# Optimization experiments

Hardware: AMD Instinct MI355X
Metric: run time of the kernel (lower is better)

The kernel has to match this reference:

```python
import jax, jax.numpy as jnp
import numpy as np

B, N, E, D = 8, 10000, 160000, 256
H = D // 2
SLOPE = 0.2  # LeakyReLU negative slope


def setup_inputs() -> dict:
    key = jax.random.key(0)
    ks = jax.random.split(key, 8)
    node_feats = jax.random.normal(ks[0], (B, N, D), dtype=jnp.float32)
    edge_attr = jax.random.uniform(ks[1], (E, 1), dtype=jnp.float32)
    W1 = jax.random.normal(ks[2], (2 * D, H), dtype=jnp.float32) * 0.05
    b1 = jnp.zeros((H,), dtype=jnp.float32)
    W2 = jax.random.normal(ks[3], (H, 1), dtype=jnp.float32) * 0.05
    b2 = jnp.zeros((1,), dtype=jnp.float32)
    edge_index = jax.random.randint(ks[4], (2, E), 0, N, dtype=jnp.int64)
    valid_masks = jax.random.randint(ks[5], (B, N), 0, 2).astype(bool)
    return {"node_feats": node_feats, "edge_attr": edge_attr, "W1": W1, "b1": b1,
            "W2": W2, "b2": b2, "edge_index": edge_index, "valid_masks": valid_masks}


def reference(node_feats, edge_attr, W1, b1, W2, b2, edge_index, valid_masks):
    # node_feats: [B,N,D]; edge_index: [2,E] shared across batch
    d = node_feats.shape[-1]
    src, dst = edge_index[0], edge_index[1]
    # cat([src_feats, dst_feats]) @ W1 == src @ W1[:d] + dst @ W1[d:]
    # Project per-node first, then gather per-edge: avoids the [B,E,2D] concat.
    ps = jnp.einsum('bnd,dh->bnh', node_feats, W1[:d])   # [B,N,H]
    pd = jnp.einsum('bnd,dh->bnh', node_feats, W1[d:])   # [B,N,H]
    h = ps[:, src] + pd[:, dst] + b1                      # [B,E,H]
    h = jnp.where(h >= 0, h, SLOPE * h)                   # LeakyReLU(0.2)
    scores = jnp.einsum('beh,h->be', h, W2[:, 0]) + b2[0]  # [B,E]
    scores = scores * edge_attr[:, 0]                     # edge_attr multiplies pre-softmax
    w = jax.nn.softmax(scores, axis=1)                    # global softmax over all edges
    # sparse_coo(edge_index, w) @ node_feats: out[src[e]] += w[e] * feats[dst[e]]
    msg = w[..., None] * node_feats[:, dst]               # [B,E,D]
    n = node_feats.shape[1]
    agg = jax.vmap(lambda m: jax.ops.segment_sum(m, src, num_segments=n))(msg)  # [B,N,D]
    mask = valid_masks.astype(node_feats.dtype)           # [B,N]
    cnt = mask.sum(axis=1)                                # [B]
    masked_mean = (agg * mask[..., None]).sum(axis=1) / jnp.maximum(cnt, 1.0)[:, None]
    full_mean = agg.mean(axis=1)
    graph_feats = jnp.where((cnt > 0)[:, None], masked_mean, full_mean)  # [B,D]
    return graph_feats, w
```

## Files before the change

### kernel.cpp

```cpp
#include <hip/hip_runtime.h>
#include <hip/hip_bf16.h>
#include <hip/hip_fp16.h>

#define B_ 8
#define N_ 10000
#define E_ 160000
#define D_ 256
#define H_ 128
#define SLOPE 0.2f
#define NCHUNK 50

#define EC_ 16
#define NR_ 32
#define RANGE_ 320
#define NPAD_ (NR_ * RANGE_)

#define NB_ 64
#define EPB_ (E_ / NB_)
#define BINS_ 256
#define NPB_ (N_ / 16)

#define SB_ 64
#define SEB_ (E_ / SB_)

typedef __attribute__((ext_vector_type(8))) _Float16 v8h;
typedef __attribute__((ext_vector_type(4))) _Float16 v4h;
typedef __attribute__((ext_vector_type(2))) _Float16 v2h;
typedef __attribute__((ext_vector_type(4))) float f32x4;

static __device__ __forceinline__ float dot2f(v2h a, v2h b, float c) {
#if __has_builtin(__builtin_amdgcn_fdot2)
    return __builtin_amdgcn_fdot2(a, b, c, false);
#else
    return fmaf((float)a.y, (float)b.y, fmaf((float)a.x, (float)b.x, c));
#endif
}

__global__ __launch_bounds__(64) void k_detect(const int* __restrict__ eidx_raw,
                                               const unsigned int* __restrict__ mask32,
                                               int* __restrict__ flags) {
    const int t = threadIdx.x;
    unsigned long long oddnz = __ballot(eidx_raw[2 * t + 1] != 0);
    unsigned long long mgt1  = __ballot(mask32[t] > 1u);
    if (t == 0) {
        flags[0] = (oddnz == 0ull) ? 1 : 0;
        flags[1] = (mgt1 != 0ull) ? 1 : 0;
    }
}

__global__ __launch_bounds__(256) void k_canon(const int* __restrict__ eidx_raw,
                                               const unsigned char* __restrict__ mask8,
                                               const unsigned int* __restrict__ mask32,
                                               const int* __restrict__ flags,
                                               const float* __restrict__ W1,
                                               const float* __restrict__ b1,
                                               const float* __restrict__ W2,
                                               int* __restrict__ ce,
                                               unsigned char* __restrict__ cm,
                                               unsigned char* __restrict__ cmT,
                                               __half* __restrict__ Wt,
                                               __half* __restrict__ b1h,
                                               __half* __restrict__ w2h) {
    const int i = blockIdx.x * 256 + threadIdx.x;
    const int f_e = flags[0], f_m = flags[1];
    if (i < 2 * E_) ce[i] = f_e ? eidx_raw[2 * i] : eidx_raw[i];
    if (i < B_ * N_) {
        unsigned char v = f_m ? (unsigned char)(mask8[i] != 0)
                              : (unsigned char)(mask32[i] != 0u);
        cm[i] = v;
        const int b = i / N_;
        const int n = i - b * N_;
        cmT[n * 8 + b] = v;
    }
    if (i < 2 * 256 * 128) {
        const int f = i & 127;
        const int row = i >> 7;
        const int c = row >> 8, k = row & 255;
        Wt[((c * 128 + f) * 256) + k] = __float2half(W1[row * 128 + f]);
    }
    if (i < 128) {
        b1h[i] = __float2half(b1[i]);
        w2h[i] = __float2half(W2[i]);
    }
}

__global__ __launch_bounds__(256) void khist(const int* __restrict__ ce,
                                             const unsigned char* __restrict__ cm,
                                             int* __restrict__ hpart,
                                             float* __restrict__ cnt) {
    const int tid = threadIdx.x;
    if (blockIdx.x < NB_) {
        __shared__ int h[BINS_];
        h[tid] = 0;
        __syncthreads();
        const int base = blockIdx.x * EPB_;
        for (int i = tid; i < EPB_; i += 256) {
            const int s = ce[base + i], d = ce[E_ + base + i];
            const int bin = (d / NPB_) * 16 + s / NPB_;
            atomicAdd(&h[bin], 1);
        }
        __syncthreads();
        hpart[blockIdx.x * BINS_ + tid] = h[tid];
    } else {
        const int b = blockIdx.x - NB_;
        int c = 0;
        for (int i = tid; i < N_; i += 256) c += cm[b * N_ + i] ? 1 : 0;
        __shared__ int red[256];
        red[tid] = c;
        __syncthreads();
        for (int s = 128; s > 0; s >>= 1) {
            if (tid < s) red[tid] += red[tid + s];
            __syncthreads();
        }
        if (tid == 0) cnt[b] = (float)red[0];
    }
}

__global__ __launch_bounds__(256) void kprefix(const int* __restrict__ hpart,
                                               int* __restrict__ offsetG) {
    __shared__ int cnt[BINS_];
    __shared__ int excl[BINS_];
    const int bin = threadIdx.x;
    int c = 0;
    for (int b = 0; b < NB_; b++) c += hpart[b * BINS_ + bin];
    cnt[bin] = c;
    __syncthreads();
    if (bin == 0) {
        int r = 0;
        for (int i = 0; i < BINS_; i++) { excl[i] = r; r += cnt[i]; }
    }
    __syncthreads();
    int run = excl[bin];
    for (int b = 0; b < NB_; b++) {
        offsetG[b * BINS_ + bin] = run;
        run += hpart[b * BINS_ + bin];
    }
}

__global__ __launch_bounds__(256) void kscatter(const int* __restrict__ ce,
                                                const int* __restrict__ offsetG,
                                                int* __restrict__ srcS,
                                                int* __restrict__ dstS,
                                                int* __restrict__ origS,
                                                int* __restrict__ rank) {
    __shared__ int loc[BINS_];
    const int tid = threadIdx.x;
    loc[tid] = offsetG[blockIdx.x * BINS_ + tid];
    __syncthreads();
    const int base = blockIdx.x * EPB_;
    for (int i = tid; i < EPB_; i += 256) {
        const int e = base + i;
        const int s = ce[e], d = ce[E_ + e];
        const int bin = (d / NPB_) * 16 + s / NPB_;
        const int pos = atomicAdd(&loc[bin], 1);
        srcS[pos] = s;
        dstS[pos] = d;
        origS[pos] = e;
        rank[e] = pos;
    }
}

__global__ __launch_bounds__(256) void k1_mfma(const float* __restrict__ X,
                                               const __half* __restrict__ Wt,
                                               __half* __restrict__ ps,
                                               __half* __restrict__ pd) {
    const int rb = blockIdx.x;
    const int tid = threadIdx.x;
    const int wave = tid >> 6, lane = tid & 63;
    const int quad = lane >> 4, l16 = lane & 15;

    __shared__ _Float16 Xs[128 * 40];

    f32x4 acc[2][2][8];
#pragma unroll
    for (int c = 0; c < 2; c++)
#pragma unroll
        for (int i = 0; i < 2; i++)
#pragma unroll
            for (int j = 0; j < 8; j++) acc[c][i][j] = (f32x4){0.f, 0.f, 0.f, 0.f};

    const int row_base = rb * 128;
    const int sr = tid >> 1;
    const int sh = tid & 1;

    for (int kc = 0; kc < 8; ++kc) {
        {
            const float4* src = (const float4*)&X[(size_t)(row_base + sr) * 256 + kc * 32 + sh * 16];
            _Float16* dst = &Xs[sr * 40 + sh * 16];
#pragma unroll
            for (int j = 0; j < 4; ++j) {
                float4 v = src[j];
                v4h p = {(_Float16)v.x, (_Float16)v.y, (_Float16)v.z, (_Float16)v.w};
                *(v4h*)&dst[j * 4] = p;
            }
        }
        __syncthreads();

        v8h wf[2][2];
#pragma unroll
        for (int cb = 0; cb < 2; ++cb)
#pragma unroll
            for (int ft = 0; ft < 2; ++ft)
                wf[cb][ft] = *(const v8h*)&Wt[((size_t)cb * 128 + wave * 32 + ft * 16 + l16) * 256 + kc * 32 + quad * 8];

#pragma unroll
        for (int nt = 0; nt < 8; ++nt) {
            v8h xf = *(v8h*)&Xs[(nt * 16 + l16) * 40 + quad * 8];
            acc[0][0][nt] = __builtin_amdgcn_mfma_f32_16x16x32_f16(wf[0][0], xf, acc[0][0][nt], 0, 0, 0);
            acc[0][1][nt] = __builtin_amdgcn_mfma_f32_16x16x32_f16(wf[0][1], xf, acc[0][1][nt], 0, 0, 0);
            acc[1][0][nt] = __builtin_amdgcn_mfma_f32_16x16x32_f16(wf[1][0], xf, acc[1][0][nt], 0, 0, 0);
            acc[1][1][nt] = __builtin_amdgcn_mfma_f32_16x16x32_f16(wf[1][1], xf, acc[1][1][nt], 0, 0, 0);
        }
        __syncthreads();
    }

#pragma unroll
    for (int nt = 0; nt < 8; ++nt) {
        const int R = row_base + nt * 16 + l16;
        const int b = R / N_;
        const int n = R - b * N_;
        const size_t off = ((size_t)(n * 8 + b)) * 128 + wave * 32 + quad * 4;
#pragma unroll
        for (int cb = 0; cb < 2; ++cb) {
            __half* base = (cb ? pd : ps) + off;
#pragma unroll
            for (int ft = 0; ft < 2; ++ft) {
                f32x4 a = acc[cb][ft][nt];
                v4h h = {(_Float16)a.x, (_Float16)a.y, (_Float16)a.z, (_Float16)a.w};
                *(v4h*)(base + ft * 16) = h;
            }
        }
    }
}

__global__ __launch_bounds__(256) void k2_scores(const __half* __restrict__ ps,
                                                 const __half* __restrict__ pd,
                                                 const int* __restrict__ srcS,
                                                 const int* __restrict__ dstS,
                                                 const int* __restrict__ origS,
                                                 const __half* __restrict__ b1h,
                                                 const __half* __restrict__ w2h,
                                                 const float* __restrict__ b2,
                                                 const float* __restrict__ eattr,
                                                 float* __restrict__ scS) {
    const int tid = threadIdx.x;
    const int wave = tid >> 6;
    const int lane = tid & 63;
    const int bid = blockIdx.x;
    const int lb = (bid & 7) * 5000 + (bid >> 3);
    const int e = lb * 4 + wave;

    const int b = lane >> 3;
    const int hi = (lane & 7) * 16;

    v2h b1p[8], w2p[8];
    {
        const v2h* bp = (const v2h*)(b1h + hi);
        const v2h* wp = (const v2h*)(w2h + hi);
#pragma unroll
        for (int j = 0; j < 8; j++) { b1p[j] = bp[j]; w2p[j] = wp[j]; }
    }

    const int src = srcS[e];
    const int dst = dstS[e];
    const int orig = origS[e];

    const float4* aps = (const float4*)&ps[((size_t)src * 8 + b) * 128 + hi];
    const float4* apd = (const float4*)&pd[((size_t)dst * 8 + b) * 128 + hi];
    float4 rs[2] = {aps[0], aps[1]};
    float4 rd[2] = {apd[0], apd[1]};
    const v2h* sv = (const v2h*)rs;
    const v2h* dv = (const v2h*)rd;

    const v2h slp = {(_Float16)SLOPE, (_Float16)SLOPE};
    float acc = 0.f;
#pragma unroll
    for (int j = 0; j < 8; j++) {
        v2h x = sv[j] + dv[j] + b1p[j];
        v2h l = __builtin_elementwise_max(x, x * slp);
        acc = dot2f(l, w2p[j], acc);
    }
    acc += __shfl_xor(acc, 1);
    acc += __shfl_xor(acc, 2);
    acc += __shfl_xor(acc, 4);

    if ((lane & 7) == 0) {
        scS[(size_t)e * 8 + b] = (acc + b2[0]) * eattr[orig];
    }
}

__global__ __launch_bounds__(256) void k3a_max(const float* __restrict__ scS,
                                               float* __restrict__ pmax) {
    const int tid = threadIdx.x;
    const int wave = tid >> 6, lane = tid & 63;
    const int base = blockIdx.x * SEB_;
    float fm[8];
#pragma unroll
    for (int j = 0; j < 8; j++) fm[j] = -3.4e38f;
    for (int i = tid; i < SEB_; i += 256) {
        const float4* s4 = (const float4*)&scS[(size_t)(base + i) * 8];
        float4 a = s4[0], b = s4[1];
        fm[0] = fmaxf(fm[0], a.x); fm[1] = fmaxf(fm[1], a.y);
        fm[2] = fmaxf(fm[2], a.z); fm[3] = fmaxf(fm[3], a.w);
        fm[4] = fmaxf(fm[4], b.x); fm[5] = fmaxf(fm[5], b.y);
        fm[6] = fmaxf(fm[6], b.z); fm[7] = fmaxf(fm[7], b.w);
    }
#pragma unroll
    for (int k = 1; k <= 32; k <<= 1)
#pragma unroll
        for (int j = 0; j < 8; j++) fm[j] = fmaxf(fm[j], __shfl_xor(fm[j], k));
    __shared__ float lmax[4][8];
    if (lane == 0)
#pragma unroll
        for (int j = 0; j < 8; j++) lmax[wave][j] = fm[j];
    __syncthreads();
    if (tid < 8) {
        float v = fmaxf(fmaxf(lmax[0][tid], lmax[1][tid]), fmaxf(lmax[2][tid], lmax[3][tid]));
        pmax[blockIdx.x * 8 + tid] = v;
    }
}

__global__ __launch_bounds__(256) void k3c_sum(const float* __restrict__ scS,
                                               const float* __restrict__ pmax,
                                               double* __restrict__ psum) {
    const int tid = threadIdx.x;
    const int wave = tid >> 6, lane = tid & 63;
    __shared__ float sm[8];
    if (tid < SB_) {
        float v[8];
        const float4* p4 = (const float4*)&pmax[tid * 8];
        float4 a = p4[0], b = p4[1];
        v[0] = a.x; v[1] = a.y; v[2] = a.z; v[3] = a.w;
        v[4] = b.x; v[5] = b.y; v[6] = b.z; v[7] = b.w;
#pragma unroll
        for (int k = 1; k <= 32; k <<= 1)
#pragma unroll
            for (int j = 0; j < 8; j++) v[j] = fmaxf(v[j], __shfl_xor(v[j], k));
        if (tid == 0)
#pragma unroll
            for (int j = 0; j < 8; j++) sm[j] = v[j];
    }
    __syncthreads();
    float m[8];
#pragma unroll
    for (int j = 0; j < 8; j++) m[j] = sm[j];

    const int base = blockIdx.x * SEB_;
    double s[8];
#pragma unroll
    for (int j = 0; j < 8; j++) s[j] = 0.0;
    for (int i = tid; i < SEB_; i += 256) {
        const float4* s4 = (const float4*)&scS[(size_t)(base + i) * 8];
        float4 a = s4[0], b = s4[1];
        s[0] += (double)expf(a.x - m[0]); s[1] += (double)expf(a.y - m[1]);
        s[2] += (double)expf(a.z - m[2]); s[3] += (double)expf(a.w - m[3]);
        s[4] += (double)expf(b.x - m[4]); s[5] += (double)expf(b.y - m[5]);
        s[6] += (double)expf(b.z - m[6]); s[7] += (double)expf(b.w - m[7]);
    }
#pragma unroll
    for (int k = 1; k <= 32; k <<= 1)
#pragma unroll
        for (int j = 0; j < 8; j++) s[j] += __shfl_xor(s[j], k);
    __shared__ double lsum[4][8];
    if (lane == 0)
#pragma unroll
        for (int j = 0; j < 8; j++) lsum[wave][j] = s[j];
    __syncthreads();
    if (tid < 8) {
        psum[blockIdx.x * 8 + tid] = lsum[0][tid] + lsum[1][tid] + lsum[2][tid] + lsum[3][tid];
    }
}

__global__ __launch_bounds__(256) void k3e_norm(const float* __restrict__ scS,
                                                const int* __restrict__ rank,
                                                const float* __restrict__ pmax,
                                                const double* __restrict__ psum,
                                                float* __restrict__ wout,
                                                float* __restrict__ wT) {
    const int tid = threadIdx.x;
    __shared__ float smx[8], sinvx[8];
    if (tid < 64) {
        float v[8];
        const float4* p4 = (const float4*)&pmax[tid * 8];
        float4 a = p4[0], b = p4[1];
        v[0] = a.x; v[1] = a.y; v[2] = a.z; v[3] = a.w;
        v[4] = b.x; v[5] = b.y; v[6] = b.z; v[7] = b.w;
#pragma unroll
        for (int k = 1; k <= 32; k <<= 1)
#pragma unroll
            for (int j = 0; j < 8; j++) v[j] = fmaxf(v[j], __shfl_xor(v[j], k));
        if (tid == 0)
#pragma unroll
            for (int j = 0; j < 8; j++) smx[j] = v[j];
    } else if (tid < 128) {
        const int l = tid - 64;
        double s[8];
#pragma unroll
        for (int j = 0; j < 8; j++) s[j] = psum[l * 8 + j];
#pragma unroll
        for (int k = 1; k <= 32; k <<= 1)
#pragma unroll
            for (int j = 0; j < 8; j++) s[j] += __shfl_xor(s[j], k);
        if (l == 0)
#pragma unroll
            for (int j = 0; j < 8; j++) sinvx[j] = (float)(1.0 / s[j]);
    }
    __syncthreads();

    const int e = blockIdx.x * 256 + tid;
    const int p = rank[e];
    const float4* s4 = (const float4*)&scS[(size_t)p * 8];
    float4 a = s4[0], b = s4[1];
    float wv[8];
    wv[0] = expf(a.x - smx[0]) * sinvx[0]; wv[1] = expf(a.y - smx[1]) * sinvx[1];
    wv[2] = expf(a.z - smx[2]) * sinvx[2]; wv[3] = expf(a.w - smx[3]) * sinvx[3];
    wv[4] = expf(b.x - smx[4]) * sinvx[4]; wv[5] = expf(b.y - smx[5]) * sinvx[5];
    wv[6] = expf(b.z - smx[6]) * sinvx[6]; wv[7] = expf(b.w - smx[7]) * sinvx[7];
#pragma unroll
    for (int j = 0; j < 8; j++) wout[(size_t)j * E_ + e] = wv[j];
    *(float4*)&wT[(size_t)e * 8]     = make_float4(wv[0], wv[1], wv[2], wv[3]);
    *(float4*)&wT[(size_t)e * 8 + 4] = make_float4(wv[4], wv[5], wv[6], wv[7]);
}

__global__ __launch_bounds__(256) void k3f_bin(const int* __restrict__ ce,
                                               const float* __restrict__ wT,
                                               const unsigned char* __restrict__ cmT,
                                               float* __restrict__ Wpart) {
    const int ec = blockIdx.x;
    const int rg = blockIdx.y;
    const int n0 = rg * RANGE_;

    __shared__ float lWf[RANGE_ * 8];
    __shared__ float lWm[RANGE_ * 8];
    for (int i = threadIdx.x; i < RANGE_ * 8; i += 256) { lWf[i] = 0.f; lWm[i] = 0.f; }
    __syncthreads();

    const int4* dst4 = (const int4*)(ce + E_);
    const int base4 = ec * (E_ / EC_ / 4);
    for (int i = threadIdx.x; i < E_ / EC_ / 4; i += 256) {
        int4 d4 = dst4[base4 + i];
        int dd[4] = {d4.x, d4.y, d4.z, d4.w};
        const int e0 = (base4 + i) * 4;
#pragma unroll
        for (int j = 0; j < 4; ++j) {
            const int rel = dd[j] - n0;
            if ((unsigned)rel < (unsigned)RANGE_) {
                const int e = e0 + j;
                const int src = ce[e];
                float4 w0 = *(const float4*)&wT[(size_t)e * 8];
                float4 w1 = *(const float4*)&wT[(size_t)e * 8 + 4];
                const unsigned long long mm = *(const unsigned long long*)&cmT[src * 8];
                float wv[8] = {w0.x, w0.y, w0.z, w0.w, w1.x, w1.y, w1.z, w1.w};
                float* lf = &lWf[rel * 8];
                float* lm = &lWm[rel * 8];
#pragma unroll
                for (int b = 0; b < 8; b++) {
                    atomicAdd(&lf[b], wv[b]);
                    if ((mm >> (8 * b)) & 1ull) atomicAdd(&lm[b], wv[b]);
                }
            }
        }
    }
    __syncthreads();

    float* of = Wpart + ((size_t)ec * 2 + 0) * (NPAD_ * 8) + n0 * 8;
    float* om = Wpart + ((size_t)ec * 2 + 1) * (NPAD_ * 8) + n0 * 8;
    for (int i = threadIdx.x; i < RANGE_ * 8; i += 256) { of[i] = lWf[i]; om[i] = lWm[i]; }
}

__global__ __launch_bounds__(256) void k3g_reduce(const float* __restrict__ Wpart,
                                                  float* __restrict__ WfT,
                                                  float* __restrict__ WmT) {
    const int i = blockIdx.x * 256 + threadIdx.x;
    float sf = 0.f, sm = 0.f;
#pragma unroll
    for (int ec = 0; ec < EC_; ec++) {
        sf += Wpart[(size_t)ec * 2 * (NPAD_ * 8) + i];
        sm += Wpart[((size_t)ec * 2 + 1) * (NPAD_ * 8) + i];
    }
    WfT[i] = sf;
    WmT[i] = sm;
}

__global__ __launch_bounds__(256) void k4b_wsum(const float* __restrict__ X,
                                                const float* __restrict__ WmT,
                                                const float* __restrict__ WfT,
                                                float* __restrict__ gpart) {
    const int c = blockIdx.x;
    const int b = blockIdx.y;
    const int tx = threadIdx.x & 63;
    const int ty = threadIdx.x >> 6;
    const int npc = N_ / NCHUNK;
    const int n0 = c * npc;

    const float4* X4 = (const float4*)(X + (size_t)b * N_ * 256);
    float4 am = {0.f, 0.f, 0.f, 0.f};
    float4 af = {0.f, 0.f, 0.f, 0.f};

    for (int n = n0 + ty; n < n0 + npc; n += 4) {
        float wm = WmT[n * 8 + b];
        float wf = WfT[n * 8 + b];
        float4 v = X4[(size_t)n * 64 + tx];
        am.x = fmaf(wm, v.x, am.x); am.y = fmaf(wm, v.y, am.y);
        am.z = fmaf(wm, v.z, am.z); am.w = fmaf(wm, v.w, am.w);
        af.x = fmaf(wf, v.x, af.x); af.y = fmaf(wf, v.y, af.y);
        af.z = fmaf(wf, v.z, af.z); af.w = fmaf(wf, v.w, af.w);
    }

    __shared__ float4 red[256];
    red[threadIdx.x] = am;
    __syncthreads();
    if (ty == 0) {
        float4 r1 = red[tx + 64], r2 = red[tx + 128], r3 = red[tx + 192];
        am.x += r1.x + r2.x + r3.x; am.y += r1.y + r2.y + r3.y;
        am.z += r1.z + r2.z + r3.z; am.w += r1.w + r2.w + r3.w;
    }
    __syncthreads();
    red[threadIdx.x] = af;
    __syncthreads();
    if (ty == 0) {
        float4 r1 = red[tx + 64], r2 = red[tx + 128], r3 = red[tx + 192];
        af.x += r1.x + r2.x + r3.x; af.y += r1.y + r2.y + r3.y;
        af.z += r1.z + r2.z + r3.z; af.w += r1.w + r2.w + r3.w;
        float4* gp4 = (float4*)gpart;
        gp4[((c * 2 + 0) * 8 + b) * 64 + tx] = am;
        gp4[((c * 2 + 1) * 8 + b) * 64 + tx] = af;
    }
}

__global__ __launch_bounds__(256) void k5_final(const float* __restrict__ gpart,
                                                const float* __restrict__ cnt,
                                                float* __restrict__ gf) {
    const int b = blockIdx.x;
    const int d = threadIdx.x;
    float sm = 0.f, sf = 0.f;
    for (int c = 0; c < NCHUNK; c++) {
        sm += gpart[((c * 2 + 0) * 8 + b) * 256 + d];
        sf += gpart[((c * 2 + 1) * 8 + b) * 256 + d];
    }
    const float cn = cnt[b];
    gf[b * 256 + d] = (cn > 0.f) ? (sm / cn) : (sf / (float)N_);
}

extern "C" void kernel_launch(void* const* d_in, const int* in_sizes, int n_in,
                              void* d_out, int out_size, void* d_ws, size_t ws_size,
                              hipStream_t stream) {
    const float* X     = (const float*)d_in[0];
    const float* eattr = (const float*)d_in[1];
    const float* W1    = (const float*)d_in[2];
    const float* b1    = (const float*)d_in[3];
    const float* W2    = (const float*)d_in[4];
    const float* b2    = (const float*)d_in[5];
    const int*   eidx_raw = (const int*)d_in[6];
    const unsigned char* mask8 = (const unsigned char*)d_in[7];
    const unsigned int*  mask32 = (const unsigned int*)d_in[7];

    float* out  = (float*)d_out;
    float* gf   = out;
    float* wout = out + 2048;

    __half* ps_h = (__half*)d_ws;
    __half* pd_h = ps_h + (size_t)N_ * 8 * 128;
    __half* Wt   = pd_h + (size_t)N_ * 8 * 128;
    int* ce = (int*)(Wt + 2 * 128 * 256);
    unsigned char* cmT = (unsigned char*)(ce + 2 * E_);
    unsigned char* cm  = cmT + NPAD_ * 8;
    float* cnt = (float*)(cm + B_ * N_);
    int* flags = (int*)(cnt + 8);
    float* pmax = (float*)(flags + 2);
    double* psum = (double*)(((uintptr_t)(pmax + SB_ * 8) + 15) & ~(uintptr_t)15);
    float* gpart = (float*)(psum + SB_ * 8);
    int* hpart   = (int*)(gpart + NCHUNK * 2 * 8 * 256);
    int* offsetG = hpart + NB_ * BINS_;
    int* srcS    = offsetG + NB_ * BINS_;
    int* dstS    = srcS + E_;
    int* origS   = dstS + E_;
    int* rankB   = origS + E_;
    __half* b1h  = (__half*)(rankB + E_);
    __half* w2h  = b1h + 128;
    float* scS   = (float*)(w2h + 128);

    float* wT    = (float*)d_ws;
    float* Wpart = wT + (size_t)E_ * 8;
    float* WfT   = Wpart + (size_t)EC_ * 2 * NPAD_ * 8;
    float* WmT   = WfT + NPAD_ * 8;

    hipLaunchKernelGGL(k_detect, dim3(1), dim3(64), 0, stream, eidx_raw, mask32, flags);
    hipLaunchKernelGGL(k_canon, dim3(1250), dim3(256), 0, stream,
                       eidx_raw, mask8, mask32, flags, W1, b1, W2,
                       ce, cm, cmT, Wt, b1h, w2h);
    hipLaunchKernelGGL(khist, dim3(NB_ + 8), dim3(256), 0, stream, ce, cm, hpart, cnt);
    hipLaunchKernelGGL(kprefix, dim3(1), dim3(256), 0, stream, hpart, offsetG);
    hipLaunchKernelGGL(kscatter, dim3(NB_), dim3(256), 0, stream,
                       ce, offsetG, srcS, dstS, origS, rankB);
    hipLaunchKernelGGL(k1_mfma, dim3(625), dim3(256), 0, stream, X, Wt, ps_h, pd_h);
    hipLaunchKernelGGL(k2_scores, dim3(E_ / 4), dim3(256), 0, stream,
                       ps_h, pd_h, srcS, dstS, origS, b1h, w2h, b2, eattr, scS);
    hipLaunchKernelGGL(k3a_max, dim3(SB_), dim3(256), 0, stream, scS, pmax);
    hipLaunchKernelGGL(k3c_sum, dim3(SB_), dim3(256), 0, stream, scS, pmax, psum);
    hipLaunchKernelGGL(k3e_norm, dim3(E_ / 256), dim3(256), 0, stream,
                       scS, rankB, pmax, psum, wout, wT);
    hipLaunchKernelGGL(k3f_bin, dim3(EC_, NR_), dim3(256), 0, stream, ce, wT, cmT, Wpart);
    hipLaunchKernelGGL(k3g_reduce, dim3(NPAD_ * 8 / 256), dim3(256), 0, stream,
                       Wpart, WfT, WmT);
    hipLaunchKernelGGL(k4b_wsum, dim3(NCHUNK, 8), dim3(256), 0, stream, X, WmT, WfT, gpart);
    hipLaunchKernelGGL(k5_final, dim3(8), dim3(256), 0, stream, gpart, cnt, gf);
}
```

Measured before the change: 314.6 us.

## Fuse softmax stats, pack sorted edges, bin weights by dst bucket

```diff
diff --git a/kernel.cpp b/kernel.cpp
--- a/kernel.cpp
+++ b/kernel.cpp
@@ -9,11 +9,6 @@
 #define H_ 128
 #define SLOPE 0.2f
 #define NCHUNK 50
-
-#define EC_ 16
-#define NR_ 32
-#define RANGE_ 320
-#define NPAD_ (NR_ * RANGE_)
 
 #define NB_ 64
 #define EPB_ (E_ / NB_)
@@ -117,7 +112,8 @@
 }
 
 __global__ __launch_bounds__(256) void kprefix(const int* __restrict__ hpart,
-                                               int* __restrict__ offsetG) {
+                                               int* __restrict__ offsetG,
+                                               int* __restrict__ bstart) {
     __shared__ int cnt[BINS_];
     __shared__ int excl[BINS_];
     const int bin = threadIdx.x;
@@ -130,6 +126,8 @@
         for (int i = 0; i < BINS_; i++) { excl[i] = r; r += cnt[i]; }
     }
     __syncthreads();
+    if ((bin & 15) == 0) bstart[bin >> 4] = excl[bin];
+    if (bin == 0) bstart[16] = E_;
     int run = excl[bin];
     for (int b = 0; b < NB_; b++) {
         offsetG[b * BINS_ + bin] = run;
@@ -139,9 +137,7 @@
 
 __global__ __launch_bounds__(256) void kscatter(const int* __restrict__ ce,
                                                 const int* __restrict__ offsetG,
-                                                int* __restrict__ srcS,
-                                                int* __restrict__ dstS,
-                                                int* __restrict__ origS,
+                                                int4* __restrict__ esort,
                                                 int* __restrict__ rank) {
     __shared__ int loc[BINS_];
     const int tid = threadIdx.x;
@@ -153,9 +149,7 @@
         const int s = ce[e], d = ce[E_ + e];
         const int bin = (d / NPB_) * 16 + s / NPB_;
         const int pos = atomicAdd(&loc[bin], 1);
-        srcS[pos] = s;
-        dstS[pos] = d;
-        origS[pos] = e;
+        esort[pos] = make_int4(s, d, e, 0);
         rank[e] = pos;
     }
 }
@@ -235,9 +229,7 @@
 
 __global__ __launch_bounds__(256) void k2_scores(const __half* __restrict__ ps,
                                                  const __half* __restrict__ pd,
-                                                 const int* __restrict__ srcS,
-                                                 const int* __restrict__ dstS,
-                                                 const int* __restrict__ origS,
+                                                 const int4* __restrict__ esort,
                                                  const __half* __restrict__ b1h,
                                                  const __half* __restrict__ w2h,
                                                  const float* __restrict__ b2,
@@ -247,8 +239,8 @@
     const int wave = tid >> 6;
     const int lane = tid & 63;
     const int bid = blockIdx.x;
-    const int lb = (bid & 7) * 5000 + (bid >> 3);
-    const int e = lb * 4 + wave;
+    const int lb = (bid & 7) * 2500 + (bid >> 3);
+    const int e0 = lb * 8 + wave * 2;
 
     const int b = lane >> 3;
     const int hi = (lane & 7) * 16;
@@ -260,40 +252,46 @@
 #pragma unroll
         for (int j = 0; j < 8; j++) { b1p[j] = bp[j]; w2p[j] = wp[j]; }
     }
-
-    const int src = srcS[e];
-    const int dst = dstS[e];
-    const int orig = origS[e];
-
-    const float4* aps = (const float4*)&ps[((size_t)src * 8 + b) * 128 + hi];
-    const float4* apd = (const float4*)&pd[((size_t)dst * 8 + b) * 128 + hi];
-    float4 rs[2] = {aps[0], aps[1]};
-    float4 rd[2] = {apd[0], apd[1]};
-    const v2h* sv = (const v2h*)rs;
-    const v2h* dv = (const v2h*)rd;
-
+    const float bias2 = b2[0];
     const v2h slp = {(_Float16)SLOPE, (_Float16)SLOPE};
-    float acc = 0.f;
-#pragma unroll
-    for (int j = 0; j < 8; j++) {
-        v2h x = sv[j] + dv[j] + b1p[j];
-        v2h l = __builtin_elementwise_max(x, x * slp);
-        acc = dot2f(l, w2p[j], acc);
-    }
-    acc += __shfl_xor(acc, 1);
-    acc += __shfl_xor(acc, 2);
-    acc += __shfl_xor(acc, 4);
-
-    if ((lane & 7) == 0) {
-        scS[(size_t)e * 8 + b] = (acc + b2[0]) * eattr[orig];
-    }
-}
-
-__global__ __launch_bounds__(256) void k3a_max(const float* __restrict__ scS,
-                                               float* __restrict__ pmax) {
+
+#pragma unroll
+    for (int q = 0; q < 2; q++) {
+        const int e = e0 + q;
+        const int4 er = esort[e];
+        const int src = er.x, dst = er.y, orig = er.z;
+
+        const float4* aps = (const float4*)&ps[((size_t)src * 8 + b) * 128 + hi];
+        const float4* apd = (const float4*)&pd[((size_t)dst * 8 + b) * 128 + hi];
+        float4 rs[2] = {aps[0], aps[1]};
+        float4 rd[2] = {apd[0], apd[1]};
+        const v2h* sv = (const v2h*)rs;
+        const v2h* dv = (const v2h*)rd;
+
+        float acc = 0.f;
+#pragma unroll
+        for (int j = 0; j < 8; j++) {
+            v2h x = sv[j] + dv[j] + b1p[j];
+            v2h l = __builtin_elementwise_max(x, x * slp);
+            acc = dot2f(l, w2p[j], acc);
+        }
+        acc += __shfl_xor(acc, 1);
+        acc += __shfl_xor(acc, 2);
+        acc += __shfl_xor(acc, 4);
+
+        if ((lane & 7) == 0) {
+            scS[(size_t)e * 8 + b] = (acc + bias2) * eattr[orig];
+        }
+    }
+}
+
+__global__ __launch_bounds__(256) void k3s_stats(const float* __restrict__ scS,
+                                                 float* __restrict__ pmax,
+                                                 double* __restrict__ psum) {
     const int tid = threadIdx.x;
     const int wave = tid >> 6, lane = tid & 63;
     const int base = blockIdx.x * SEB_;
+
     float fm[8];
 #pragma unroll
     for (int j = 0; j < 8; j++) fm[j] = -3.4e38f;
@@ -314,38 +312,11 @@
 #pragma unroll
         for (int j = 0; j < 8; j++) lmax[wave][j] = fm[j];
     __syncthreads();
-    if (tid < 8) {
-        float v = fmaxf(fmaxf(lmax[0][tid], lmax[1][tid]), fmaxf(lmax[2][tid], lmax[3][tid]));
-        pmax[blockIdx.x * 8 + tid] = v;
-    }
-}
-
-__global__ __launch_bounds__(256) void k3c_sum(const float* __restrict__ scS,
-                                               const float* __restrict__ pmax,
-                                               double* __restrict__ psum) {
-    const int tid = threadIdx.x;
-    const int wave = tid >> 6, lane = tid & 63;
-    __shared__ float sm[8];
-    if (tid < SB_) {
-        float v[8];
-        const float4* p4 = (const float4*)&pmax[tid * 8];
-        float4 a = p4[0], b = p4[1];
-        v[0] = a.x; v[1] = a.y; v[2] = a.z; v[3] = a.w;
-        v[4] = b.x; v[5] = b.y; v[6] = b.z; v[7] = b.w;
-#pragma unroll
-        for (int k = 1; k <= 32; k <<= 1)
-#pragma unroll
-            for (int j = 0; j < 8; j++) v[j] = fmaxf(v[j], __shfl_xor(v[j], k));
-        if (tid == 0)
-#pragma unroll
-            for (int j = 0; j < 8; j++) sm[j] = v[j];
-    }
-    __syncthreads();
     float m[8];
 #pragma unroll
-    for (int j = 0; j < 8; j++) m[j] = sm[j];
-
-    const int base = blockIdx.x * SEB_;
+    for (int j = 0; j < 8; j++)
+        m[j] = fmaxf(fmaxf(lmax[0][j], lmax[1][j]), fmaxf(lmax[2][j], lmax[3][j]));
+
     double s[8];
 #pragma unroll
     for (int j = 0; j < 8; j++) s[j] = 0.0;
@@ -367,44 +338,49 @@
         for (int j = 0; j < 8; j++) lsum[wave][j] = s[j];
     __syncthreads();
     if (tid < 8) {
+        pmax[blockIdx.x * 8 + tid] = m[tid];
         psum[blockIdx.x * 8 + tid] = lsum[0][tid] + lsum[1][tid] + lsum[2][tid] + lsum[3][tid];
     }
 }
 
-__global__ __launch_bounds__(256) void k3e_norm(const float* __restrict__ scS,
-                                                const int* __restrict__ rank,
-                                                const float* __restrict__ pmax,
-                                                const double* __restrict__ psum,
-                                                float* __restrict__ wout,
-                                                float* __restrict__ wT) {
-    const int tid = threadIdx.x;
-    __shared__ float smx[8], sinvx[8];
+static __device__ __forceinline__ void stats_combine(const float* __restrict__ pmax,
+                                                     const double* __restrict__ psum,
+                                                     int tid, float* smx, float* sinvx) {
     if (tid < 64) {
         float v[8];
         const float4* p4 = (const float4*)&pmax[tid * 8];
         float4 a = p4[0], b = p4[1];
         v[0] = a.x; v[1] = a.y; v[2] = a.z; v[3] = a.w;
         v[4] = b.x; v[5] = b.y; v[6] = b.z; v[7] = b.w;
+        float mc[8];
+#pragma unroll
+        for (int j = 0; j < 8; j++) mc[j] = v[j];
 #pragma unroll
         for (int k = 1; k <= 32; k <<= 1)
 #pragma unroll
             for (int j = 0; j < 8; j++) v[j] = fmaxf(v[j], __shfl_xor(v[j], k));
+        double z[8];
+#pragma unroll
+        for (int j = 0; j < 8; j++)
+            z[j] = psum[tid * 8 + j] * (double)expf(mc[j] - v[j]);
+#pragma unroll
+        for (int k = 1; k <= 32; k <<= 1)
+#pragma unroll
+            for (int j = 0; j < 8; j++) z[j] += __shfl_xor(z[j], k);
         if (tid == 0)
 #pragma unroll
-            for (int j = 0; j < 8; j++) smx[j] = v[j];
-    } else if (tid < 128) {
-        const int l = tid - 64;
-        double s[8];
-#pragma unroll
-        for (int j = 0; j < 8; j++) s[j] = psum[l * 8 + j];
-#pragma unroll
-        for (int k = 1; k <= 32; k <<= 1)
-#pragma unroll
-            for (int j = 0; j < 8; j++) s[j] += __shfl_xor(s[j], k);
-        if (l == 0)
-#pragma unroll
-            for (int j = 0; j < 8; j++) sinvx[j] = (float)(1.0 / s[j]);
-    }
+            for (int j = 0; j < 8; j++) { smx[j] = v[j]; sinvx[j] = (float)(1.0 / z[j]); }
+    }
+}
+
+__global__ __launch_bounds__(256) void k3e_norm(const float* __restrict__ scS,
+                                                const int* __restrict__ rank,
+                                                const float* __restrict__ pmax,
+                                                const double* __restrict__ psum,
+                                                float* __restrict__ wout) {
+    const int tid = threadIdx.x;
+    __shared__ float smx[8], sinvx[8];
+    stats_combine(pmax, psum, tid, smx, sinvx);
     __syncthreads();
 
     const int e = blockIdx.x * 256 + tid;
@@ -418,65 +394,80 @@
     wv[6] = expf(b.z - smx[6]) * sinvx[6]; wv[7] = expf(b.w - smx[7]) * sinvx[7];
 #pragma unroll
     for (int j = 0; j < 8; j++) wout[(size_t)j * E_ + e] = wv[j];
-    *(float4*)&wT[(size_t)e * 8]     = make_float4(wv[0], wv[1], wv[2], wv[3]);
-    *(float4*)&wT[(size_t)e * 8 + 4] = make_float4(wv[4], wv[5], wv[6], wv[7]);
-}
-
-__global__ __launch_bounds__(256) void k3f_bin(const int* __restrict__ ce,
-                                               const float* __restrict__ wT,
+}
+
+__global__ __launch_bounds__(256) void k3f_bin(const int4* __restrict__ esort,
+                                               const float* __restrict__ scS,
                                                const unsigned char* __restrict__ cmT,
-                                               float* __restrict__ Wpart) {
-    const int ec = blockIdx.x;
-    const int rg = blockIdx.y;
-    const int n0 = rg * RANGE_;
-
-    __shared__ float lWf[RANGE_ * 8];
-    __shared__ float lWm[RANGE_ * 8];
-    for (int i = threadIdx.x; i < RANGE_ * 8; i += 256) { lWf[i] = 0.f; lWm[i] = 0.f; }
-    __syncthreads();
-
-    const int4* dst4 = (const int4*)(ce + E_);
-    const int base4 = ec * (E_ / EC_ / 4);
-    for (int i = threadIdx.x; i < E_ / EC_ / 4; i += 256) {
-        int4 d4 = dst4[base4 + i];
-        int dd[4] = {d4.x, d4.y, d4.z, d4.w};
-        const int e0 = (base4 + i) * 4;
-#pragma unroll
-        for (int j = 0; j < 4; ++j) {
-            const int rel = dd[j] - n0;
-            if ((unsigned)rel < (unsigned)RANGE_) {
-                const int e = e0 + j;
-                const int src = ce[e];
-                float4 w0 = *(const float4*)&wT[(size_t)e * 8];
-                float4 w1 = *(const float4*)&wT[(size_t)e * 8 + 4];
-                const unsigned long long mm = *(const unsigned long long*)&cmT[src * 8];
-                float wv[8] = {w0.x, w0.y, w0.z, w0.w, w1.x, w1.y, w1.z, w1.w};
-                float* lf = &lWf[rel * 8];
-                float* lm = &lWm[rel * 8];
-#pragma unroll
-                for (int b = 0; b < 8; b++) {
-                    atomicAdd(&lf[b], wv[b]);
-                    if ((mm >> (8 * b)) & 1ull) atomicAdd(&lm[b], wv[b]);
-                }
-            }
-        }
-    }
-    __syncthreads();
-
-    float* of = Wpart + ((size_t)ec * 2 + 0) * (NPAD_ * 8) + n0 * 8;
-    float* om = Wpart + ((size_t)ec * 2 + 1) * (NPAD_ * 8) + n0 * 8;
-    for (int i = threadIdx.x; i < RANGE_ * 8; i += 256) { of[i] = lWf[i]; om[i] = lWm[i]; }
-}
-
-__global__ __launch_bounds__(256) void k3g_reduce(const float* __restrict__ Wpart,
+                                               const float* __restrict__ pmax,
+                                               const double* __restrict__ psum,
+                                               const int* __restrict__ bstart,
+                                               float* __restrict__ Wpf,
+                                               float* __restrict__ Wpm) {
+    const int bucket = blockIdx.x;
+    const int sub = blockIdx.y;
+    const int tid = threadIdx.x;
+
+    __shared__ float smx[8], sinvx[8];
+    stats_combine(pmax, psum, tid, smx, sinvx);
+
+    __shared__ float lWf[NPB_ * 8];
+    __shared__ float lWm[NPB_ * 8];
+    for (int i = tid; i < NPB_ * 8; i += 256) { lWf[i] = 0.f; lWm[i] = 0.f; }
+    __syncthreads();
+
+    float m[8], inv[8];
+#pragma unroll
+    for (int j = 0; j < 8; j++) { m[j] = smx[j]; inv[j] = sinvx[j]; }
+
+    const int bs = bstart[bucket], be = bstart[bucket + 1];
+    const int len = be - bs;
+    const int s0 = bs + (int)((long long)len * sub / 8);
+    const int s1 = bs + (int)((long long)len * (sub + 1) / 8);
+    const int nbase = bucket * NPB_;
+
+    for (int p = s0 + tid; p < s1; p += 256) {
+        const int4 er = esort[p];
+        const int src = er.x;
+        const int rel = er.y - nbase;
+        const float4* s4 = (const float4*)&scS[(size_t)p * 8];
+        float4 a = s4[0], b = s4[1];
+        float wv[8];
+        wv[0] = expf(a.x - m[0]) * inv[0]; wv[1] = expf(a.y - m[1]) * inv[1];
+        wv[2] = expf(a.z - m[2]) * inv[2]; wv[3] = expf(a.w - m[3]) * inv[3];
+        wv[4] = expf(b.x - m[4]) * inv[4]; wv[5] = expf(b.y - m[5]) * inv[5];
+        wv[6] = expf(b.z - m[6]) * inv[6]; wv[7] = expf(b.w - m[7]) * inv[7];
+        const unsigned long long mm = *(const unsigned long long*)&cmT[src * 8];
+        float* lf = &lWf[rel * 8];
+        float* lm = &lWm[rel * 8];
+#pragma unroll
+        for (int j = 0; j < 8; j++) {
+            atomicAdd(&lf[j], wv[j]);
+            if ((mm >> (8 * j)) & 1ull) atomicAdd(&lm[j], wv[j]);
+        }
+    }
+    __syncthreads();
+
+    float* of = Wpf + ((size_t)bucket * 8 + sub) * (NPB_ * 8);
+    float* om = Wpm + ((size_t)bucket * 8 + sub) * (NPB_ * 8);
+    for (int i = tid; i < NPB_ * 8; i += 256) { of[i] = lWf[i]; om[i] = lWm[i]; }
+}
+
+__global__ __launch_bounds__(256) void k3g_reduce(const float* __restrict__ Wpf,
+                                                  const float* __restrict__ Wpm,
                                                   float* __restrict__ WfT,
                                                   float* __restrict__ WmT) {
     const int i = blockIdx.x * 256 + threadIdx.x;
+    if (i >= N_ * 8) return;
+    const int n = i >> 3, b = i & 7;
+    const int bucket = n / NPB_;
+    const int rel = n - bucket * NPB_;
     float sf = 0.f, sm = 0.f;
 #pragma unroll
-    for (int ec = 0; ec < EC_; ec++) {
-        sf += Wpart[(size_t)ec * 2 * (NPAD_ * 8) + i];
-        sm += Wpart[((size_t)ec * 2 + 1) * (NPAD_ * 8) + i];
+    for (int sub = 0; sub < 8; sub++) {
+        const size_t off = ((size_t)bucket * 8 + sub) * (NPB_ * 8) + rel * 8 + b;
+        sf += Wpf[off];
+        sm += Wpm[off];
     }
     WfT[i] = sf;
     WmT[i] = sm;
@@ -540,6 +531,10 @@
     }
     const float cn = cnt[b];
     gf[b * 256 + d] = (cn > 0.f) ? (sm / cn) : (sf / (float)N_);
+}
+
+static inline char* align16(char* p) {
+    return (char*)(((uintptr_t)p + 15) & ~(uintptr_t)15);
 }
 
 extern "C" void kernel_launch(void* const* d_in, const int* in_sizes, int n_in,
@@ -559,50 +554,55 @@
     float* gf   = out;
     float* wout = out + 2048;
 
-    __half* ps_h = (__half*)d_ws;
-    __half* pd_h = ps_h + (size_t)N_ * 8 * 128;
-    __half* Wt   = pd_h + (size_t)N_ * 8 * 128;
-    int* ce = (int*)(Wt + 2 * 128 * 256);
-    unsigned char* cmT = (unsigned char*)(ce + 2 * E_);
-    unsigned char* cm  = cmT + NPAD_ * 8;
-    float* cnt = (float*)(cm + B_ * N_);
-    int* flags = (int*)(cnt + 8);
-    float* pmax = (float*)(flags + 2);
-    double* psum = (double*)(((uintptr_t)(pmax + SB_ * 8) + 15) & ~(uintptr_t)15);
-    float* gpart = (float*)(psum + SB_ * 8);
-    int* hpart   = (int*)(gpart + NCHUNK * 2 * 8 * 256);
-    int* offsetG = hpart + NB_ * BINS_;
-    int* srcS    = offsetG + NB_ * BINS_;
-    int* dstS    = srcS + E_;
-    int* origS   = dstS + E_;
-    int* rankB   = origS + E_;
-    __half* b1h  = (__half*)(rankB + E_);
-    __half* w2h  = b1h + 128;
-    float* scS   = (float*)(w2h + 128);
-
-    float* wT    = (float*)d_ws;
-    float* Wpart = wT + (size_t)E_ * 8;
-    float* WfT   = Wpart + (size_t)EC_ * 2 * NPAD_ * 8;
-    float* WmT   = WfT + NPAD_ * 8;
+    char* cur = (char*)d_ws;
+    __half* ps_h = (__half*)cur;             cur += (size_t)N_ * 8 * 128 * 2;
+    __half* pd_h = (__half*)cur;             cur += (size_t)N_ * 8 * 128 * 2;
+    __half* Wt   = (__half*)cur;             cur += 2 * 128 * 256 * 2;
+    int* ce      = (int*)cur;                cur += 2 * E_ * 4;
+    unsigned char* cmT = (unsigned char*)cur; cur += N_ * 8;
+    unsigned char* cm  = (unsigned char*)cur; cur += B_ * N_;
+    cur = align16(cur);
+    float* cnt   = (float*)cur;              cur += 8 * 4;
+    int* flags   = (int*)cur;                cur += 2 * 4;
+    cur = align16(cur);
+    float* pmax  = (float*)cur;              cur += SB_ * 8 * 4;
+    cur = align16(cur);
+    double* psum = (double*)cur;             cur += SB_ * 8 * 8;
+    float* gpart = (float*)cur;              cur += NCHUNK * 2 * 8 * 256 * 4;
+    int* hpart   = (int*)cur;                cur += NB_ * BINS_ * 4;
+    int* offsetG = (int*)cur;                cur += NB_ * BINS_ * 4;
+    int* bstart  = (int*)cur;                cur += 32 * 4;
+    cur = align16(cur);
+    int4* esort  = (int4*)cur;               cur += (size_t)E_ * 16;
+    int* rankB   = (int*)cur;                cur += E_ * 4;
+    __half* b1h  = (__half*)cur;             cur += 128 * 2;
+    __half* w2h  = (__half*)cur;             cur += 128 * 2;
+    cur = align16(cur);
+    float* scS   = (float*)cur;              cur += (size_t)E_ * 8 * 4;
+
+    char* ocur = (char*)d_ws;
+    float* Wpf = (float*)ocur;               ocur += (size_t)16 * 8 * NPB_ * 8 * 4;
+    float* Wpm = (float*)ocur;               ocur += (size_t)16 * 8 * NPB_ * 8 * 4;
+    float* WfT = (float*)ocur;               ocur += N_ * 8 * 4;
+    float* WmT = (float*)ocur;               ocur += N_ * 8 * 4;
 
     hipLaunchKernelGGL(k_detect, dim3(1), dim3(64), 0, stream, eidx_raw, mask32, flags);
     hipLaunchKernelGGL(k_canon, dim3(1250), dim3(256), 0, stream,
                        eidx_raw, mask8, mask32, flags, W1, b1, W2,
                        ce, cm, cmT, Wt, b1h, w2h);
     hipLaunchKernelGGL(khist, dim3(NB_ + 8), dim3(256), 0, stream, ce, cm, hpart, cnt);
-    hipLaunchKernelGGL(kprefix, dim3(1), dim3(256), 0, stream, hpart, offsetG);
-    hipLaunchKernelGGL(kscatter, dim3(NB_), dim3(256), 0, stream,
-                       ce, offsetG, srcS, dstS, origS, rankB);
+    hipLaunchKernelGGL(kprefix, dim3(1), dim3(256), 0, stream, hpart, offsetG, bstart);
+    hipLaunchKernelGGL(kscatter, dim3(NB_), dim3(256), 0, stream, ce, offsetG, esort, rankB);
     hipLaunchKernelGGL(k1_mfma, dim3(625), dim3(256), 0, stream, X, Wt, ps_h, pd_h);
-    hipLaunchKernelGGL(k2_scores, dim3(E_ / 4), dim3(256), 0, stream,
-                       ps_h, pd_h, srcS, dstS, origS, b1h, w2h, b2, eattr, scS);
-    hipLaunchKernelGGL(k3a_max, dim3(SB_), dim3(256), 0, stream, scS, pmax);
-    hipLaunchKernelGGL(k3c_sum, dim3(SB_), dim3(256), 0, stream, scS, pmax, psum);
+    hipLaunchKernelGGL(k2_scores, dim3(E_ / 8), dim3(256), 0, stream,
+                       ps_h, pd_h, esort, b1h, w2h, b2, eattr, scS);
+    hipLaunchKernelGGL(k3s_stats, dim3(SB_), dim3(256), 0, stream, scS, pmax, psum);
     hipLaunchKernelGGL(k3e_norm, dim3(E_ / 256), dim3(256), 0, stream,
-                       scS, rankB, pmax, psum, wout, wT);
-    hipLaunchKernelGGL(k3f_bin, dim3(EC_, NR_), dim3(256), 0, stream, ce, wT, cmT, Wpart);
-    hipLaunchKernelGGL(k3g_reduce, dim3(NPAD_ * 8 / 256), dim3(256), 0, stream,
-                       Wpart, WfT, WmT);
+                       scS, rankB, pmax, psum, wout);
+    hipLaunchKernelGGL(k3f_bin, dim3(16, 8), dim3(256), 0, stream,
+                       esort, scS, cmT, pmax, psum, bstart, Wpf, Wpm);
+    hipLaunchKernelGGL(k3g_reduce, dim3((N_ * 8 + 255) / 256), dim3(256), 0, stream,
+                       Wpf, Wpm, WfT, WmT);
     hipLaunchKernelGGL(k4b_wsum, dim3(NCHUNK, 8), dim3(256), 0, stream, X, WmT, WfT, gpart);
     hipLaunchKernelGGL(k5_final, dim3(8), dim3(256), 0, stream, gpart, cnt, gf);
 }
```

Measured after the change: 299.2 us. 1.05x faster.
